# Kernel optimization log

Measured on AMD Instinct MI355X. Metric: run time of the kernel, lower is better.

## Reference

```python
import jax, jax.numpy as jnp
import numpy as np

MARGIN = 0.2  # self.margin; temperature is unused in the original forward


def setup_inputs() -> dict:
    key = jax.random.key(0)
    k1, k2 = jax.random.split(key)
    B, D, NUM_CLASSES = 512, 256, 10
    features = jax.random.normal(k1, (B, D), dtype=jnp.float32)
    labels = jax.random.randint(k2, (B,), 0, NUM_CLASSES, dtype=jnp.int32)
    return {"features": features, "labels": labels}


def reference(features, labels):
    B = features.shape[0]
    sim = features @ features.T  # [B, B]

    eq = (labels[:, None] == labels[None, :])
    pos_mask = eq.astype(sim.dtype) * (1.0 - jnp.eye(B, dtype=sim.dtype))  # diag zeroed
    neg_mask = 1.0 - eq.astype(sim.dtype)

    # For anchor row i, pos j, neg k: relu(margin + sim[i,k] - sim[i,j])
    hinge = jax.nn.relu(MARGIN + sim[:, None, :] - sim[:, :, None])  # [B, Bpos, Bneg]
    loss_sum = jnp.einsum('ijk,ij,ik->', hinge, pos_mask, neg_mask)

    pos_cnt = pos_mask.sum(axis=1)  # per-row positive counts
    neg_cnt = neg_mask.sum(axis=1)
    valid = (pos_cnt > 0) & (neg_cnt > 0)
    num_valid = valid.sum().astype(sim.dtype)

    # Original bug faithfully reproduced: denominator uses the LAST row's
    # pos/neg counts (pos_sim/neg_sim leak out of the python loop).
    denom = num_valid * pos_cnt[-1] * neg_cnt[-1]
    return jnp.where(denom > 0, loss_sum / denom, jnp.zeros((), sim.dtype))
```

## Files before the change

### kernel.cpp

```cpp
#include <hip/hip_runtime.h>

#define B 512
#define D 256
#define NCLS 10
#define MARGIN 0.2f
#define THREADS 256
#define NWAVES (THREADS / 64)
#define ROWS 2
#define NBLOCKS (B / ROWS)
#define DT 32
#define NDT (D / DT)
#define JS 514

__global__ __launch_bounds__(THREADS) void fused_loss_kernel(
    const float* __restrict__ F, const int* __restrict__ labels,
    float* __restrict__ out)
{
    __shared__ float ldsT[DT * JS];
    __shared__ float fi[ROWS][D];
    __shared__ float simrow[ROWS][B];
    __shared__ int   lbl[B];
    __shared__ float pos_vals[B];
    __shared__ float neg_vals[B];
    __shared__ int   cnt[2];
    __shared__ int   hist[NCLS];
    __shared__ float wred[NWAVES];
    __shared__ int   vred[NWAVES];

    const int t    = threadIdx.x;
    const int lane = t & 63;
    const int w    = t >> 6;
    const int i0   = blockIdx.x * ROWS;

    lbl[t]       = labels[t];
    lbl[t + 256] = labels[t + 256];
    if (t < NCLS) hist[t] = 0;
    if (t < (ROWS * D) / 4)
        ((float4*)fi)[t] = ((const float4*)(F + (size_t)i0 * D))[t];
    __syncthreads();

    atomicAdd(&hist[lbl[t]], 1);
    atomicAdd(&hist[lbl[t + 256]], 1);

    float acc00 = 0.f, acc01 = 0.f, acc10 = 0.f, acc11 = 0.f;
    const float4* Fv = (const float4*)F;
    for (int tile = 0; tile < NDT; ++tile) {
        const int dt4 = tile * (DT / 4);
#pragma unroll
        for (int k = 0; k < (B * DT / 4) / THREADS; ++k) {
            const int g   = t + THREADS * k;
            const int row = g >> 3;
            const int m   = g & 7;
            const float4 v = Fv[row * (D / 4) + dt4 + m];
            ldsT[(4 * m + 0) * JS + row] = v.x;
            ldsT[(4 * m + 1) * JS + row] = v.y;
            ldsT[(4 * m + 2) * JS + row] = v.z;
            ldsT[(4 * m + 3) * JS + row] = v.w;
        }
        __syncthreads();
        const int dt = tile * DT;
#pragma unroll
        for (int e4 = 0; e4 < DT / 4; ++e4) {
            const float4 a0 = *(const float4*)&fi[0][dt + 4 * e4];
            const float4 a1 = *(const float4*)&fi[1][dt + 4 * e4];
#pragma unroll
            for (int q = 0; q < 4; ++q) {
                const float2 x = *(const float2*)&ldsT[(4 * e4 + q) * JS + 2 * t];
                const float a0q = q == 0 ? a0.x : q == 1 ? a0.y : q == 2 ? a0.z : a0.w;
                const float a1q = q == 0 ? a1.x : q == 1 ? a1.y : q == 2 ? a1.z : a1.w;
                acc00 = fmaf(a0q, x.x, acc00);
                acc01 = fmaf(a0q, x.y, acc01);
                acc10 = fmaf(a1q, x.x, acc10);
                acc11 = fmaf(a1q, x.y, acc11);
            }
        }
        __syncthreads();
    }
    *(float2*)&simrow[0][2 * t] = make_float2(acc00, acc01);
    *(float2*)&simrow[1][2 * t] = make_float2(acc10, acc11);
    __syncthreads();

    {
        const int ca = hist[lbl[t]];
        const int cb = hist[lbl[t + 256]];
        const unsigned long long ma = __ballot(ca >= 2 && ca <= B - 1);
        const unsigned long long mb = __ballot(cb >= 2 && cb <= B - 1);
        if (lane == 0) vred[w] = __popcll(ma) + __popcll(mb);
    }

    float local = 0.f;
    for (int r = 0; r < ROWS; ++r) {
        const int i  = i0 + r;
        const int li = lbl[i];
        if (t == 0) { cnt[0] = 0; cnt[1] = 0; }
        __syncthreads();
#pragma unroll
        for (int h = 0; h < 2; ++h) {
            const int j = 2 * t + h;
            const bool active = (j != i);
            const bool ispos  = active && (lbl[j] == li);
            const bool isneg  = active && (lbl[j] != li);
            const unsigned long long mp = __ballot(ispos);
            const unsigned long long mn = __ballot(isneg);
            int basep = 0, basen = 0;
            if (lane == 0) {
                basep = atomicAdd(&cnt[0], __popcll(mp));
                basen = atomicAdd(&cnt[1], __popcll(mn));
            }
            basep = __shfl(basep, 0, 64);
            basen = __shfl(basen, 0, 64);
            const unsigned long long below = (1ull << lane) - 1ull;
            if (ispos) pos_vals[basep + __popcll(mp & below)] = simrow[r][j];
            if (isneg) neg_vals[basen + __popcll(mn & below)] = simrow[r][j];
        }
        __syncthreads();
        const int P = cnt[0], N = cnt[1];
        for (int pi = 0; pi < P; ++pi) {
            const float pv = pos_vals[pi] - MARGIN;
            for (int ni = t; ni < N; ni += THREADS) {
                const float v = neg_vals[ni] - pv;
                local += (v > 0.f) ? v : 0.f;
            }
        }
        __syncthreads();
    }

#pragma unroll
    for (int off = 32; off > 0; off >>= 1)
        local += __shfl_down(local, off, 64);
    if (lane == 0) wred[w] = local;
    __syncthreads();
    if (t == 0) {
        float s = 0.f;
        int   nv = 0;
#pragma unroll
        for (int k = 0; k < NWAVES; ++k) { s += wred[k]; nv += vred[k]; }
        const int   clast = hist[lbl[B - 1]];
        const float denom = (float)nv * (float)(clast - 1) * (float)(B - clast);
        atomicAdd(out, (denom > 0.f) ? s / denom : 0.f);
    }
}

extern "C" void kernel_launch(void* const* d_in, const int* in_sizes, int n_in,
                              void* d_out, int out_size, void* d_ws, size_t ws_size,
                              hipStream_t stream) {
    const float* F      = (const float*)d_in[0];
    const int*   labels = (const int*)d_in[1];
    float* out = (float*)d_out;
    (void)d_ws; (void)ws_size;

    fused_loss_kernel<<<NBLOCKS, THREADS, 0, stream>>>(F, labels, out);
}
```

Baseline: 83.65 us.

## Use 1024 threads, one per (row, column) pair, and process both anchor rows concurrently

Raises the block to 1024 threads so each thread computes one similarity entry, for one of the two anchor rows against one column. Feature tiles are stored row-major with a small padded stride instead of a transposed layout. Both rows are compacted into their own positive and negative lists at once, which removes the per-row loop and its barriers. Each thread keeps one negative value in a register and loops over the positives. The larger block raises register pressure and may lower occupancy, and each thread does fewer FMAs per shared-memory load.

Measured after the change: 71.55 us. 1.17x faster.

```diff
diff --git a/kernel.cpp b/kernel.cpp
--- a/kernel.cpp
+++ b/kernel.cpp
@@ -4,25 +4,25 @@
 #define D 256
 #define NCLS 10
 #define MARGIN 0.2f
-#define THREADS 256
+#define THREADS 1024
 #define NWAVES (THREADS / 64)
 #define ROWS 2
 #define NBLOCKS (B / ROWS)
 #define DT 32
 #define NDT (D / DT)
-#define JS 514
+#define JS 36
 
 __global__ __launch_bounds__(THREADS) void fused_loss_kernel(
     const float* __restrict__ F, const int* __restrict__ labels,
     float* __restrict__ out)
 {
-    __shared__ float ldsT[DT * JS];
+    __shared__ float ldsR[B * JS];
     __shared__ float fi[ROWS][D];
     __shared__ float simrow[ROWS][B];
     __shared__ int   lbl[B];
-    __shared__ float pos_vals[B];
-    __shared__ float neg_vals[B];
-    __shared__ int   cnt[2];
+    __shared__ float pos_vals[ROWS][B];
+    __shared__ float neg_vals[ROWS][B];
+    __shared__ int   cnt[ROWS][2];
     __shared__ int   hist[NCLS];
     __shared__ float wred[NWAVES];
     __shared__ int   vred[NWAVES];
@@ -31,19 +31,22 @@
     const int lane = t & 63;
     const int w    = t >> 6;
     const int i0   = blockIdx.x * ROWS;
+    const int r    = t >> 9;
+    const int j    = t & (B - 1);
 
-    lbl[t]       = labels[t];
-    lbl[t + 256] = labels[t + 256];
+    if (t < B)    lbl[t] = labels[t];
     if (t < NCLS) hist[t] = 0;
     if (t < (ROWS * D) / 4)
         ((float4*)fi)[t] = ((const float4*)(F + (size_t)i0 * D))[t];
+    if (t < ROWS * 2) ((int*)cnt)[t] = 0;
     __syncthreads();
 
-    atomicAdd(&hist[lbl[t]], 1);
-    atomicAdd(&hist[lbl[t + 256]], 1);
+    if (t < B) atomicAdd(&hist[lbl[t]], 1);
 
-    float acc00 = 0.f, acc01 = 0.f, acc10 = 0.f, acc11 = 0.f;
-    const float4* Fv = (const float4*)F;
+    float acc = 0.f;
+    const float4* Fv   = (const float4*)F;
+    const float*  base = &ldsR[j * JS];
+    const float*  fr   = fi[r];
     for (int tile = 0; tile < NDT; ++tile) {
         const int dt4 = tile * (DT / 4);
 #pragma unroll
@@ -51,78 +54,59 @@
             const int g   = t + THREADS * k;
             const int row = g >> 3;
             const int m   = g & 7;
-            const float4 v = Fv[row * (D / 4) + dt4 + m];
-            ldsT[(4 * m + 0) * JS + row] = v.x;
-            ldsT[(4 * m + 1) * JS + row] = v.y;
-            ldsT[(4 * m + 2) * JS + row] = v.z;
-            ldsT[(4 * m + 3) * JS + row] = v.w;
+            *(float4*)&ldsR[row * JS + 4 * m] = Fv[row * (D / 4) + dt4 + m];
         }
         __syncthreads();
         const int dt = tile * DT;
 #pragma unroll
         for (int e4 = 0; e4 < DT / 4; ++e4) {
-            const float4 a0 = *(const float4*)&fi[0][dt + 4 * e4];
-            const float4 a1 = *(const float4*)&fi[1][dt + 4 * e4];
-#pragma unroll
-            for (int q = 0; q < 4; ++q) {
-                const float2 x = *(const float2*)&ldsT[(4 * e4 + q) * JS + 2 * t];
-                const float a0q = q == 0 ? a0.x : q == 1 ? a0.y : q == 2 ? a0.z : a0.w;
-                const float a1q = q == 0 ? a1.x : q == 1 ? a1.y : q == 2 ? a1.z : a1.w;
-                acc00 = fmaf(a0q, x.x, acc00);
-                acc01 = fmaf(a0q, x.y, acc01);
-                acc10 = fmaf(a1q, x.x, acc10);
-                acc11 = fmaf(a1q, x.y, acc11);
-            }
+            const float4 a = *(const float4*)&fr[dt + 4 * e4];
+            const float4 x = *(const float4*)&base[4 * e4];
+            acc = fmaf(a.x, x.x, acc);
+            acc = fmaf(a.y, x.y, acc);
+            acc = fmaf(a.z, x.z, acc);
+            acc = fmaf(a.w, x.w, acc);
         }
         __syncthreads();
     }
-    *(float2*)&simrow[0][2 * t] = make_float2(acc00, acc01);
-    *(float2*)&simrow[1][2 * t] = make_float2(acc10, acc11);
+    simrow[r][j] = acc;
     __syncthreads();
 
     {
-        const int ca = hist[lbl[t]];
-        const int cb = hist[lbl[t + 256]];
-        const unsigned long long ma = __ballot(ca >= 2 && ca <= B - 1);
-        const unsigned long long mb = __ballot(cb >= 2 && cb <= B - 1);
-        if (lane == 0) vred[w] = __popcll(ma) + __popcll(mb);
+        bool valid = false;
+        if (t < B) { const int c = hist[lbl[t]]; valid = (c >= 2) && (c <= B - 1); }
+        const unsigned long long mv = __ballot(valid);
+        if (lane == 0) vred[w] = __popcll(mv);
     }
 
+    const int i_r = i0 + r;
+    const int li  = lbl[i_r];
+    {
+        const bool active = (j != i_r);
+        const bool ispos  = active && (lbl[j] == li);
+        const bool isneg  = active && (lbl[j] != li);
+        const unsigned long long mp = __ballot(ispos);
+        const unsigned long long mn = __ballot(isneg);
+        int basep = 0, basen = 0;
+        if (lane == 0) {
+            basep = atomicAdd(&cnt[r][0], __popcll(mp));
+            basen = atomicAdd(&cnt[r][1], __popcll(mn));
+        }
+        basep = __shfl(basep, 0, 64);
+        basen = __shfl(basen, 0, 64);
+        const unsigned long long below = (1ull << lane) - 1ull;
+        const float sv = simrow[r][j];
+        if (ispos) pos_vals[r][basep + __popcll(mp & below)] = sv;
+        if (isneg) neg_vals[r][basen + __popcll(mn & below)] = sv;
+    }
+    __syncthreads();
+
+    const int P = cnt[r][0], N = cnt[r][1];
+    const float nv_t = (j < N) ? neg_vals[r][j] : -1e30f;
     float local = 0.f;
-    for (int r = 0; r < ROWS; ++r) {
-        const int i  = i0 + r;
-        const int li = lbl[i];
-        if (t == 0) { cnt[0] = 0; cnt[1] = 0; }
-        __syncthreads();
-#pragma unroll
-        for (int h = 0; h < 2; ++h) {
-            const int j = 2 * t + h;
-            const bool active = (j != i);
-            const bool ispos  = active && (lbl[j] == li);
-            const bool isneg  = active && (lbl[j] != li);
-            const unsigned long long mp = __ballot(ispos);
-            const unsigned long long mn = __ballot(isneg);
-            int basep = 0, basen = 0;
-            if (lane == 0) {
-                basep = atomicAdd(&cnt[0], __popcll(mp));
-                basen = atomicAdd(&cnt[1], __popcll(mn));
-            }
-            basep = __shfl(basep, 0, 64);
-            basen = __shfl(basen, 0, 64);
-            const unsigned long long below = (1ull << lane) - 1ull;
-            if (ispos) pos_vals[basep + __popcll(mp & below)] = simrow[r][j];
-            if (isneg) neg_vals[basen + __popcll(mn & below)] = simrow[r][j];
-        }
-        __syncthreads();
-        const int P = cnt[0], N = cnt[1];
-        for (int pi = 0; pi < P; ++pi) {
-            const float pv = pos_vals[pi] - MARGIN;
-            for (int ni = t; ni < N; ni += THREADS) {
-                const float v = neg_vals[ni] - pv;
-                local += (v > 0.f) ? v : 0.f;
-            }
-        }
-        __syncthreads();
+    for (int pi = 0; pi < P; ++pi) {
+        const float v = nv_t - (pos_vals[r][pi] - MARGIN);
+        local += (v > 0.f) ? v : 0.f;
     }
 
 #pragma unroll
```
